# Kernel optimization log

Measured on AMD Instinct MI355X. Metric: run time of the kernel, lower is better.

## Reference

```python
import jax, jax.numpy as jnp
import numpy as np

EMBED = 1024
HEADS = 16
HEAD_DIM = EMBED // HEADS
SCALE = HEAD_DIM ** (-0.5)
LN_EPS = 1e-5


def setup_inputs() -> dict:
    key = jax.random.key(0)
    ks = jax.random.split(key, 8)
    B, N = 2, 2048
    s = EMBED ** -0.5
    return {
        "x": jax.random.normal(ks[0], (B, N, EMBED), dtype=jnp.float32),
        "ln_w": jnp.ones((EMBED,), jnp.float32),
        "ln_b": jnp.zeros((EMBED,), jnp.float32),
        "Wq": jax.random.normal(ks[1], (EMBED, EMBED), jnp.float32) * s,
        "Wk": jax.random.normal(ks[2], (EMBED, EMBED), jnp.float32) * s,
        "Wv": jax.random.normal(ks[3], (EMBED, EMBED), jnp.float32) * s,
        "Wo": jax.random.normal(ks[4], (EMBED, EMBED), jnp.float32) * s,
        "bo": jnp.zeros((EMBED,), jnp.float32),
    }


def reference(x, ln_w, ln_b, Wq, Wk, Wv, Wo, bo):
    residual = x
    # LayerNorm (pre-norm)
    mu = jnp.mean(x, axis=-1, keepdims=True)
    var = jnp.mean(jnp.square(x - mu), axis=-1, keepdims=True)
    xn = (x - mu) * jax.lax.rsqrt(var + LN_EPS) * ln_w + ln_b

    B, N, _ = xn.shape
    q = (xn @ Wq.T).reshape(B, N, HEADS, HEAD_DIM).transpose(0, 2, 1, 3)  # b h n d
    k = (xn @ Wk.T).reshape(B, N, HEADS, HEAD_DIM).transpose(0, 2, 1, 3)
    v = (xn @ Wv.T).reshape(B, N, HEADS, HEAD_DIM).transpose(0, 2, 1, 3)

    dots = jnp.einsum('bhqd,bhkd->bhqk', q, k) * SCALE
    causal = jnp.tril(jnp.ones((N, N), dtype=bool))
    dots = jnp.where(causal, dots, -jnp.inf)
    attn = jax.nn.softmax(dots, axis=-1)
    out = jnp.einsum('bhqk,bhkd->bhqd', attn, v)
    out = out.transpose(0, 2, 1, 3).reshape(B, N, EMBED)
    # dropout is identity in eval mode
    return residual + out @ Wo.T + bo
```

## Files before the change

### kernel.cpp

```cpp
#include <hip/hip_runtime.h>

#define E 1024
#define NSEQ 2048
#define HEADS 16
#define HD 64

typedef unsigned short u16;
typedef short short8 __attribute__((ext_vector_type(8)));
typedef float f32x4 __attribute__((ext_vector_type(4)));

template<bool B> struct BC { static constexpr bool v = B; };

#define GLOAD_LDS16(gp, lp)                                        \
    __builtin_amdgcn_global_load_lds(                              \
        (const __attribute__((address_space(1))) void*)(gp),       \
        (__attribute__((address_space(3))) void*)(lp), 16, 0, 0)

__device__ __forceinline__ u16 f2bf(float f) {
    union { float f; unsigned u; } v; v.f = f;
    unsigned r = v.u + 0x7fffu + ((v.u >> 16) & 1u);
    return (u16)(r >> 16);
}

__device__ __forceinline__ unsigned cvt_pk_bf16(float lo, float hi) {
    unsigned r;
    asm("v_cvt_pk_bf16_f32 %0, %1, %2" : "=v"(r) : "v"(lo), "v"(hi));
    return r;
}

__device__ __forceinline__ f32x4 mfma16(short8 a, short8 b, f32x4 c) {
    return __builtin_amdgcn_mfma_f32_16x16x32_bf16(a, b, c, 0, 0, 0);
}

__global__ __launch_bounds__(256) void prep_k(
    const float* __restrict__ Wq, const float* __restrict__ Wk,
    const float* __restrict__ Wv, const float* __restrict__ Wo,
    const float* __restrict__ X, const float* __restrict__ w,
    const float* __restrict__ bb, u16* __restrict__ Wbf, u16* __restrict__ xn)
{
    if (blockIdx.x < 4096) {
        const unsigned i = (blockIdx.x * 256u + threadIdx.x) * 4u;
        const unsigned m = i >> 20;
        const float* src = (m == 0) ? Wq : (m == 1) ? Wk : (m == 2) ? Wv : Wo;
        const float4 v = *(const float4*)(src + (i & 0xFFFFFu));
        *(uint2*)(Wbf + i) = make_uint2(
            ((unsigned)f2bf(v.x)) | (((unsigned)f2bf(v.y)) << 16),
            ((unsigned)f2bf(v.z)) | (((unsigned)f2bf(v.w)) << 16));
        return;
    }
    const int row = blockIdx.x - 4096, tid = threadIdx.x;
    const int lane = tid & 63, wave = tid >> 6;
    const float4 v = ((const float4*)(X + (size_t)row * E))[tid];
    float s = v.x + v.y + v.z + v.w;
    float s2 = v.x * v.x + v.y * v.y + v.z * v.z + v.w * v.w;
#pragma unroll
    for (int off = 1; off < 64; off <<= 1) {
        s += __shfl_xor(s, off);
        s2 += __shfl_xor(s2, off);
    }
    __shared__ float red[8];
    if (lane == 0) { red[wave] = s; red[4 + wave] = s2; }
    __syncthreads();
    s = red[0] + red[1] + red[2] + red[3];
    s2 = red[4] + red[5] + red[6] + red[7];
    const float mu = s * (1.f / 1024.f);
    float var = s2 * (1.f / 1024.f) - mu * mu;
    var = fmaxf(var, 0.f);
    const float rs = rsqrtf(var + 1e-5f);
    const float4 wv = ((const float4*)w)[tid];
    const float4 bv = ((const float4*)bb)[tid];
    u16 o0 = f2bf((v.x - mu) * rs * wv.x + bv.x);
    u16 o1 = f2bf((v.y - mu) * rs * wv.y + bv.y);
    u16 o2 = f2bf((v.z - mu) * rs * wv.z + bv.z);
    u16 o3 = f2bf((v.w - mu) * rs * wv.w + bv.w);
    *(uint2*)(xn + (size_t)row * E + tid * 4) =
        make_uint2(((unsigned)o0) | (((unsigned)o1) << 16),
                   ((unsigned)o2) | (((unsigned)o3) << 16));
}

__global__ __launch_bounds__(256) void vtrans(
    const u16* __restrict__ Vb, u16* __restrict__ VT)
{
    __shared__ u16 tl[64][65];
    const int t = threadIdx.x;
    const int ntile = blockIdx.x, bh = blockIdx.y;
    const int b = bh >> 4, h = bh & 15;
    const int n0 = ntile * 64;
    {
        const int nl = t >> 2;
        const u16* src = Vb + ((size_t)b * NSEQ + n0 + nl) * E + h * 64;
#pragma unroll
        for (int u = 0; u < 2; ++u) {
            const int d0 = (t & 3) * 16 + u * 8;
            short8 v = *(const short8*)(src + d0);
#pragma unroll
            for (int j = 0; j < 8; ++j) tl[nl][d0 + j] = (u16)v[j];
        }
    }
    __syncthreads();
    {
        const int d = t >> 2, nc = (t & 3) * 16;
        u16* dst = VT + ((size_t)bh * 64 + d) * NSEQ + n0 + nc;
#pragma unroll
        for (int u = 0; u < 2; ++u) {
            short8 o;
#pragma unroll
            for (int j = 0; j < 8; ++j) o[j] = (short)tl[nc + u * 8 + j][d];
            *(short8*)(dst + u * 8) = o;
        }
    }
}

template<int MODE>
__global__ __launch_bounds__(256) void gemm_nt(
    const u16* __restrict__ A, const u16* __restrict__ Wbase,
    u16* __restrict__ outb, float* __restrict__ outf,
    const float* __restrict__ resid, const float* __restrict__ bias)
{
    __shared__ __align__(16) unsigned char As[128 * 128];
    __shared__ __align__(16) unsigned char Bs[128 * 128];
    const int tid = threadIdx.x;
    const int lane = tid & 63, wave = tid >> 6;
    const int l15 = lane & 15, l4 = lane >> 4;
    const int wm = wave >> 1, wn = wave & 1;
    const int nt = blockIdx.x, mt = blockIdx.y, z = blockIdx.z;
    const u16* Bw = Wbase + (size_t)z * (E * (size_t)E);

    const int lrow8 = lane >> 3;
    const int lchunk = (lane & 7) ^ lrow8;
    const u16* gA = A + (size_t)(mt * 128 + lrow8) * E + lchunk * 8;
    const u16* gB = Bw + (size_t)(nt * 128 + lrow8) * E + lchunk * 8;

    f32x4 acc[4][4] = {};

    for (int kt = 0; kt < 16; ++kt) {
#pragma unroll
        for (int i = 0; i < 4; ++i) {
            const int rb = (i * 4 + wave) * 8;
            GLOAD_LDS16(gA + (size_t)rb * E + kt * 64, As + rb * 128);
            GLOAD_LDS16(gB + (size_t)rb * E + kt * 64, Bs + rb * 128);
        }
        __syncthreads();
#pragma unroll
        for (int ks = 0; ks < 2; ++ks) {
            short8 af[4], bfr[4];
#pragma unroll
            for (int i = 0; i < 4; ++i) {
                int ra = wm * 64 + i * 16 + l15;
                af[i] = *(const short8*)(As + ra * 128 + ((ks * 64 + l4 * 16) ^ ((ra & 7) << 4)));
                int rb2 = wn * 64 + i * 16 + l15;
                bfr[i] = *(const short8*)(Bs + rb2 * 128 + ((ks * 64 + l4 * 16) ^ ((rb2 & 7) << 4)));
            }
#pragma unroll
            for (int i = 0; i < 4; ++i)
#pragma unroll
                for (int j = 0; j < 4; ++j)
                    acc[i][j] = mfma16(af[i], bfr[j], acc[i][j]);
        }
        __syncthreads();
    }

    const int orow0 = mt * 128 + wm * 64, ocol0 = nt * 128 + wn * 64;
    if (MODE == 0) {
        u16* outz = outb + (size_t)z * (4096 * (size_t)E);
        const float osc = (z == 0) ? 0.18033688f : 1.0f;
#pragma unroll
        for (int i = 0; i < 4; ++i)
#pragma unroll
            for (int j = 0; j < 4; ++j)
#pragma unroll
                for (int r = 0; r < 4; ++r) {
                    int row = orow0 + i * 16 + l4 * 4 + r;
                    int col = ocol0 + j * 16 + l15;
                    outz[(size_t)row * E + col] = f2bf(acc[i][j][r] * osc);
                }
    } else {
#pragma unroll
        for (int i = 0; i < 4; ++i)
#pragma unroll
            for (int j = 0; j < 4; ++j)
#pragma unroll
                for (int r = 0; r < 4; ++r) {
                    int row = orow0 + i * 16 + l4 * 4 + r;
                    int col = ocol0 + j * 16 + l15;
                    size_t idx = (size_t)row * E + col;
                    outf[idx] = acc[i][j][r] + resid[idx] + bias[col];
                }
    }
}

__global__ __launch_bounds__(256) void attn_fwd(
    const u16* __restrict__ Q, const u16* __restrict__ K,
    const u16* __restrict__ VT, u16* __restrict__ O)
{
    __shared__ __align__(16) unsigned char Kls[2 * 16384];
    __shared__ __align__(16) unsigned char Vls[2 * 16384];
    __shared__ __align__(16) unsigned char Ps[4 * 4096];
    const int tid = threadIdx.x, lane = tid & 63, wave = tid >> 6;
    const int sub = wave >> 1, par = wave & 1;
    const int l15 = lane & 15, l4 = lane >> 4;
    const int h = blockIdx.x, y = blockIdx.y, b = blockIdx.z;
    const int jj = 31 - (int)y;
    const size_t bbase = (size_t)b * NSEQ * E + h * HD;
    const u16* vt = VT + ((size_t)(b * 16 + h) * 64) * NSEQ;

    unsigned char* Pw = Ps + wave * 4096;
    const int srowK = lane >> 3, kchunk = (lane & 7) ^ srowK;
    const int srowV = lane >> 4, vchunk = (lane & 15) ^ (((wave & 1) << 2) + srowV);

    auto stage = [&](int t, int buf) {
        const u16* Kg = K + bbase + (size_t)(t * 128) * E;
        const u16* vg = vt + t * 128;
        unsigned char* kd = Kls + buf * 16384 + wave * 1024;
        unsigned char* vd = Vls + buf * 16384 + wave * 1024;
#pragma unroll
        for (int i = 0; i < 4; ++i)
            GLOAD_LDS16(Kg + (size_t)(wave * 8 + i * 32 + srowK) * E + kchunk * 8, kd + i * 4096);
#pragma unroll
        for (int i = 0; i < 4; ++i)
            GLOAD_LDS16(vg + (size_t)(wave * 4 + i * 16 + srowV) * NSEQ + vchunk * 8, vd + i * 4096);
    };

    const int qw0 = jj * 64 + sub * 32;
    const int R = (jj >> 1) + 1;

    short8 aq[2][2];
#pragma unroll
    for (int qt = 0; qt < 2; ++qt)
#pragma unroll
        for (int ks = 0; ks < 2; ++ks)
            aq[qt][ks] = *(const short8*)(Q + bbase + (size_t)(qw0 + qt * 16 + l15) * E + ks * 32 + l4 * 8);

    f32x4 accO[2][4] = {};
    float mrow[2] = {-5e29f, -5e29f};
    float lrow[2] = {0.f, 0.f};

    stage(0, 0);
    __syncthreads();

    auto step = [&](int t, auto mc) {
        constexpr bool MASK = decltype(mc)::v;
        const int buf = t & 1;
        if (t + 1 < R) stage(t + 1, buf ^ 1);
        const unsigned char* Kc = Kls + buf * 16384;
        const unsigned char* Vc = Vls + buf * 16384;

        f32x4 s[2][4] = {};
#pragma unroll
        for (int kvt = 0; kvt < 4; ++kvt) {
            const int kr = par * 64 + kvt * 16 + l15;
#pragma unroll
            for (int ks = 0; ks < 2; ++ks) {
                short8 kfr = *(const short8*)(Kc + kr * 128 + ((ks * 64 + l4 * 16) ^ ((kr & 7) << 4)));
                s[0][kvt] = mfma16(kfr, aq[0][ks], s[0][kvt]);
                s[1][kvt] = mfma16(kfr, aq[1][ks], s[1][kvt]);
            }
        }

        if constexpr (MASK) {
#pragma unroll
            for (int qt = 0; qt < 2; ++qt) {
                const int qg = qw0 + qt * 16 + l15;
#pragma unroll
                for (int kvt = 0; kvt < 4; ++kvt)
#pragma unroll
                    for (int r = 0; r < 4; ++r) {
                        int kvg = t * 128 + par * 64 + kvt * 16 + l4 * 4 + r;
                        if (kvg > qg) s[qt][kvt][r] = -1e30f;
                    }
            }
        }

#pragma unroll
        for (int qt = 0; qt < 2; ++qt) {
            float m0 = fmaxf(fmaxf(s[qt][0][0], s[qt][0][1]), fmaxf(s[qt][0][2], s[qt][0][3]));
            float m1 = fmaxf(fmaxf(s[qt][1][0], s[qt][1][1]), fmaxf(s[qt][1][2], s[qt][1][3]));
            float m2 = fmaxf(fmaxf(s[qt][2][0], s[qt][2][1]), fmaxf(s[qt][2][2], s[qt][2][3]));
            float m3 = fmaxf(fmaxf(s[qt][3][0], s[qt][3][1]), fmaxf(s[qt][3][2], s[qt][3][3]));
            float pm = fmaxf(fmaxf(m0, m1), fmaxf(m2, m3));
            if (__any(pm > mrow[qt] + 8.f)) {
                pm = fmaxf(pm, __shfl_xor(pm, 16));
                pm = fmaxf(pm, __shfl_xor(pm, 32));
                const float mn = fmaxf(mrow[qt], pm);
                const float sc = exp2f(mrow[qt] - mn);
                mrow[qt] = mn;
                lrow[qt] *= sc;
#pragma unroll
                for (int r = 0; r < 4; ++r) {
                    float scv = __shfl(sc, l4 * 4 + r);
#pragma unroll
                    for (int dt = 0; dt < 4; ++dt) accO[qt][dt][r] *= scv;
                }
            }
            const int pr = qt * 16 + l15;
            const int sw = (l15 & 7) << 4;
#pragma unroll
            for (int kvt = 0; kvt < 4; ++kvt) {
                float p0 = exp2f(s[qt][kvt][0] - mrow[qt]);
                float p1 = exp2f(s[qt][kvt][1] - mrow[qt]);
                float p2 = exp2f(s[qt][kvt][2] - mrow[qt]);
                float p3 = exp2f(s[qt][kvt][3] - mrow[qt]);
                lrow[qt] += (p0 + p1) + (p2 + p3);
                uint2 pk = make_uint2(cvt_pk_bf16(p0, p1), cvt_pk_bf16(p2, p3));
                *(uint2*)(Pw + pr * 128 + ((kvt * 32 + l4 * 8) ^ sw)) = pk;
            }
        }

#pragma unroll
        for (int ks2 = 0; ks2 < 2; ++ks2) {
            const int cb = ks2 * 64 + l4 * 16;
            short8 pf0 = *(const short8*)(Pw + l15 * 128 + (cb ^ ((l15 & 7) << 4)));
            short8 pf1 = *(const short8*)(Pw + (16 + l15) * 128 + (cb ^ ((l15 & 7) << 4)));
#pragma unroll
            for (int dt = 0; dt < 4; ++dt) {
                const int vr = dt * 16 + l15;
                short8 vfr = *(const short8*)(Vc + vr * 256 + ((par * 128 + cb) ^ ((vr & 7) << 4)));
                accO[0][dt] = mfma16(pf0, vfr, accO[0][dt]);
                accO[1][dt] = mfma16(pf1, vfr, accO[1][dt]);
            }
        }
        __syncthreads();
    };

    for (int t = 0; t + 1 < R; ++t) step(t, BC<false>{});
    step(R - 1, BC<true>{});

    f32x4* Mg = (f32x4*)Kls;
    if (par == 1) {
        f32x4 hd;
        hd[0] = mrow[0]; hd[1] = mrow[1]; hd[2] = lrow[0]; hd[3] = lrow[1];
        Mg[(sub * 9) * 64 + lane] = hd;
#pragma unroll
        for (int qt = 0; qt < 2; ++qt)
#pragma unroll
            for (int dt = 0; dt < 4; ++dt)
                Mg[(sub * 9 + 1 + qt * 4 + dt) * 64 + lane] = accO[qt][dt];
    }
    __syncthreads();
    if (par == 0) {
        f32x4 hd = Mg[(sub * 9) * 64 + lane];
        float scA[2], scB[2];
#pragma unroll
        for (int qt = 0; qt < 2; ++qt) {
            const float mB = hd[qt], lB = hd[2 + qt];
            const float ms = fmaxf(mrow[qt], mB);
            scA[qt] = exp2f(mrow[qt] - ms);
            scB[qt] = exp2f(mB - ms);
            lrow[qt] = lrow[qt] * scA[qt] + lB * scB[qt];
        }
#pragma unroll
        for (int qt = 0; qt < 2; ++qt)
#pragma unroll
            for (int r = 0; r < 4; ++r) {
                float sa = __shfl(scA[qt], l4 * 4 + r);
                float sb = __shfl(scB[qt], l4 * 4 + r);
#pragma unroll
                for (int dt = 0; dt < 4; ++dt) {
                    f32x4 ob = Mg[(sub * 9 + 1 + qt * 4 + dt) * 64 + lane];
                    accO[qt][dt][r] = accO[qt][dt][r] * sa + ob[r] * sb;
                }
            }
        float linv[2];
#pragma unroll
        for (int qt = 0; qt < 2; ++qt) {
            float tl2 = lrow[qt];
            tl2 += __shfl_xor(tl2, 16);
            tl2 += __shfl_xor(tl2, 32);
            linv[qt] = 1.f / tl2;
        }
#pragma unroll
        for (int rt = 0; rt < 2; ++rt)
#pragma unroll
            for (int r = 0; r < 4; ++r) {
                float lq = __shfl(linv[rt], l4 * 4 + r);
                const int qg = qw0 + rt * 16 + l4 * 4 + r;
#pragma unroll
                for (int dt = 0; dt < 4; ++dt)
                    O[bbase + (size_t)qg * E + dt * 16 + l15] = f2bf(accO[rt][dt][r] * lq);
            }
    }
}

extern "C" void kernel_launch(void* const* d_in, const int* in_sizes, int n_in,
                              void* d_out, int out_size, void* d_ws, size_t ws_size,
                              hipStream_t stream)
{
    const float* x    = (const float*)d_in[0];
    const float* ln_w = (const float*)d_in[1];
    const float* ln_b = (const float*)d_in[2];
    const float* Wq   = (const float*)d_in[3];
    const float* Wk   = (const float*)d_in[4];
    const float* Wv   = (const float*)d_in[5];
    const float* Wo   = (const float*)d_in[6];
    const float* bo   = (const float*)d_in[7];
    float* out = (float*)d_out;

    u16* ws  = (u16*)d_ws;
    u16* Wbf = ws;
    u16* xn  = Wbf + (size_t)4 * 1024 * 1024;
    u16* Qb  = xn + (size_t)4096 * 1024;
    u16* Kb  = Qb + (size_t)4096 * 1024;
    u16* Vb  = Kb + (size_t)4096 * 1024;
    u16* Ob  = Vb + (size_t)4096 * 1024;
    u16* VT  = xn;

    prep_k<<<dim3(8192), dim3(256), 0, stream>>>(Wq, Wk, Wv, Wo, x, ln_w, ln_b, Wbf, xn);
    gemm_nt<0><<<dim3(8, 32, 3), dim3(256), 0, stream>>>(
        xn, Wbf, Qb, nullptr, nullptr, nullptr);
    vtrans<<<dim3(32, 32), dim3(256), 0, stream>>>(Vb, VT);
    attn_fwd<<<dim3(16, 32, 2), dim3(256), 0, stream>>>(Qb, Kb, VT, Ob);
    gemm_nt<1><<<dim3(8, 32, 1), dim3(256), 0, stream>>>(
        Ob, Wbf + (size_t)3 * 1024 * 1024, nullptr, out, x, bo);
}
```

Baseline: 122.8 us.

## Fuse V transpose into QKV GEMM epilogue and pair causal strips per attention block

The V projection epilogue now transposes its tile through LDS and writes V^T directly, which removes the separate vtrans kernel and its extra global round trip. The attention kernel launches half as many blocks, and each block processes a short and a long causal query strip (jg and 31-jg) to balance work across blocks. The costs are fewer blocks in flight for attention, a longer serial body per block, and LDS reuse in the GEMM epilogue that depends on the waitcnt ordering being correct.

```diff
diff --git a/kernel.cpp b/kernel.cpp
--- a/kernel.cpp
+++ b/kernel.cpp
@@ -8,6 +8,7 @@
 typedef unsigned short u16;
 typedef short short8 __attribute__((ext_vector_type(8)));
 typedef float f32x4 __attribute__((ext_vector_type(4)));
+typedef u16 u16x4 __attribute__((ext_vector_type(4)));
 
 template<bool B> struct BC { static constexpr bool v = B; };
 
@@ -78,43 +79,10 @@
                    ((unsigned)o2) | (((unsigned)o3) << 16));
 }
 
-__global__ __launch_bounds__(256) void vtrans(
-    const u16* __restrict__ Vb, u16* __restrict__ VT)
-{
-    __shared__ u16 tl[64][65];
-    const int t = threadIdx.x;
-    const int ntile = blockIdx.x, bh = blockIdx.y;
-    const int b = bh >> 4, h = bh & 15;
-    const int n0 = ntile * 64;
-    {
-        const int nl = t >> 2;
-        const u16* src = Vb + ((size_t)b * NSEQ + n0 + nl) * E + h * 64;
-#pragma unroll
-        for (int u = 0; u < 2; ++u) {
-            const int d0 = (t & 3) * 16 + u * 8;
-            short8 v = *(const short8*)(src + d0);
-#pragma unroll
-            for (int j = 0; j < 8; ++j) tl[nl][d0 + j] = (u16)v[j];
-        }
-    }
-    __syncthreads();
-    {
-        const int d = t >> 2, nc = (t & 3) * 16;
-        u16* dst = VT + ((size_t)bh * 64 + d) * NSEQ + n0 + nc;
-#pragma unroll
-        for (int u = 0; u < 2; ++u) {
-            short8 o;
-#pragma unroll
-            for (int j = 0; j < 8; ++j) o[j] = (short)tl[nc + u * 8 + j][d];
-            *(short8*)(dst + u * 8) = o;
-        }
-    }
-}
-
 template<int MODE>
 __global__ __launch_bounds__(256) void gemm_nt(
     const u16* __restrict__ A, const u16* __restrict__ Wbase,
-    u16* __restrict__ outb, float* __restrict__ outf,
+    u16* __restrict__ outb, u16* __restrict__ vtout, float* __restrict__ outf,
     const float* __restrict__ resid, const float* __restrict__ bias)
 {
     __shared__ __align__(16) unsigned char As[128 * 128];
@@ -162,18 +130,42 @@
 
     const int orow0 = mt * 128 + wm * 64, ocol0 = nt * 128 + wn * 64;
     if (MODE == 0) {
-        u16* outz = outb + (size_t)z * (4096 * (size_t)E);
-        const float osc = (z == 0) ? 0.18033688f : 1.0f;
-#pragma unroll
-        for (int i = 0; i < 4; ++i)
-#pragma unroll
-            for (int j = 0; j < 4; ++j)
-#pragma unroll
-                for (int r = 0; r < 4; ++r) {
-                    int row = orow0 + i * 16 + l4 * 4 + r;
-                    int col = ocol0 + j * 16 + l15;
-                    outz[(size_t)row * E + col] = f2bf(acc[i][j][r] * osc);
-                }
+        if (z == 2) {
+            unsigned char* wl = (wave < 2) ? (As + wave * 8192) : (Bs + (wave - 2) * 8192);
+#pragma unroll
+            for (int i = 0; i < 4; ++i)
+#pragma unroll
+                for (int j = 0; j < 4; ++j) {
+                    u16x4 pk;
+#pragma unroll
+                    for (int r = 0; r < 4; ++r) pk[r] = f2bf(acc[i][j][r]);
+                    const int dl = j * 16 + l15;
+                    const int boff = dl * 128 + ((i * 32 + l4 * 8) ^ ((dl & 7) << 4));
+                    *(u16x4*)(wl + boff) = pk;
+                }
+            asm volatile("s_waitcnt lgkmcnt(0)" ::: "memory");
+            const int b2 = mt >> 4, hh = nt * 2 + wn;
+            const int n0 = (mt & 15) * 128 + wm * 64;
+            u16* vrow = vtout + (size_t)((b2 * 16 + hh) * 64 + lane) * NSEQ + n0;
+#pragma unroll
+            for (int c = 0; c < 8; ++c) {
+                short8 vv = *(const short8*)(wl + lane * 128 + ((c * 16) ^ ((lane & 7) << 4)));
+                *(short8*)(vrow + c * 8) = vv;
+            }
+        } else {
+            u16* outz = outb + (size_t)z * (4096 * (size_t)E);
+            const float osc = (z == 0) ? 0.18033688f : 1.0f;
+#pragma unroll
+            for (int i = 0; i < 4; ++i)
+#pragma unroll
+                for (int j = 0; j < 4; ++j)
+#pragma unroll
+                    for (int r = 0; r < 4; ++r) {
+                        int row = orow0 + i * 16 + l4 * 4 + r;
+                        int col = ocol0 + j * 16 + l15;
+                        outz[(size_t)row * E + col] = f2bf(acc[i][j][r] * osc);
+                    }
+        }
     } else {
 #pragma unroll
         for (int i = 0; i < 4; ++i)
@@ -199,8 +191,7 @@
     const int tid = threadIdx.x, lane = tid & 63, wave = tid >> 6;
     const int sub = wave >> 1, par = wave & 1;
     const int l15 = lane & 15, l4 = lane >> 4;
-    const int h = blockIdx.x, y = blockIdx.y, b = blockIdx.z;
-    const int jj = 31 - (int)y;
+    const int h = blockIdx.x, jg = blockIdx.y, b = blockIdx.z;
     const size_t bbase = (size_t)b * NSEQ * E + h * HD;
     const u16* vt = VT + ((size_t)(b * 16 + h) * 64) * NSEQ;
 
@@ -221,164 +212,170 @@
             GLOAD_LDS16(vg + (size_t)(wave * 4 + i * 16 + srowV) * NSEQ + vchunk * 8, vd + i * 4096);
     };
 
-    const int qw0 = jj * 64 + sub * 32;
-    const int R = (jj >> 1) + 1;
-
-    short8 aq[2][2];
-#pragma unroll
-    for (int qt = 0; qt < 2; ++qt)
-#pragma unroll
-        for (int ks = 0; ks < 2; ++ks)
-            aq[qt][ks] = *(const short8*)(Q + bbase + (size_t)(qw0 + qt * 16 + l15) * E + ks * 32 + l4 * 8);
-
-    f32x4 accO[2][4] = {};
-    float mrow[2] = {-5e29f, -5e29f};
-    float lrow[2] = {0.f, 0.f};
-
-    stage(0, 0);
-    __syncthreads();
-
-    auto step = [&](int t, auto mc) {
-        constexpr bool MASK = decltype(mc)::v;
-        const int buf = t & 1;
-        if (t + 1 < R) stage(t + 1, buf ^ 1);
-        const unsigned char* Kc = Kls + buf * 16384;
-        const unsigned char* Vc = Vls + buf * 16384;
-
-        f32x4 s[2][4] = {};
-#pragma unroll
-        for (int kvt = 0; kvt < 4; ++kvt) {
-            const int kr = par * 64 + kvt * 16 + l15;
-#pragma unroll
-            for (int ks = 0; ks < 2; ++ks) {
-                short8 kfr = *(const short8*)(Kc + kr * 128 + ((ks * 64 + l4 * 16) ^ ((kr & 7) << 4)));
-                s[0][kvt] = mfma16(kfr, aq[0][ks], s[0][kvt]);
-                s[1][kvt] = mfma16(kfr, aq[1][ks], s[1][kvt]);
-            }
+    auto run_strip = [&](int jj) {
+        const int qw0 = jj * 64 + sub * 32;
+        const int R = (jj >> 1) + 1;
+
+        short8 aq[2][2];
+#pragma unroll
+        for (int qt = 0; qt < 2; ++qt)
+#pragma unroll
+            for (int ks = 0; ks < 2; ++ks)
+                aq[qt][ks] = *(const short8*)(Q + bbase + (size_t)(qw0 + qt * 16 + l15) * E + ks * 32 + l4 * 8);
+
+        f32x4 accO[2][4] = {};
+        float mrow[2] = {-5e29f, -5e29f};
+        float lrow[2] = {0.f, 0.f};
+
+        stage(0, 0);
+        __syncthreads();
+
+        auto step = [&](int t, auto mc) {
+            constexpr bool MASK = decltype(mc)::v;
+            const int buf = t & 1;
+            if (t + 1 < R) stage(t + 1, buf ^ 1);
+            const unsigned char* Kc = Kls + buf * 16384;
+            const unsigned char* Vc = Vls + buf * 16384;
+
+            f32x4 s[2][4] = {};
+#pragma unroll
+            for (int kvt = 0; kvt < 4; ++kvt) {
+                const int kr = par * 64 + kvt * 16 + l15;
+#pragma unroll
+                for (int ks = 0; ks < 2; ++ks) {
+                    short8 kfr = *(const short8*)(Kc + kr * 128 + ((ks * 64 + l4 * 16) ^ ((kr & 7) << 4)));
+                    s[0][kvt] = mfma16(kfr, aq[0][ks], s[0][kvt]);
+                    s[1][kvt] = mfma16(kfr, aq[1][ks], s[1][kvt]);
+                }
+            }
+
+            if constexpr (MASK) {
+#pragma unroll
+                for (int qt = 0; qt < 2; ++qt) {
+                    const int qg = qw0 + qt * 16 + l15;
+#pragma unroll
+                    for (int kvt = 0; kvt < 4; ++kvt)
+#pragma unroll
+                        for (int r = 0; r < 4; ++r) {
+                            int kvg = t * 128 + par * 64 + kvt * 16 + l4 * 4 + r;
+                            if (kvg > qg) s[qt][kvt][r] = -1e30f;
+                        }
+                }
+            }
+
+#pragma unroll
+            for (int qt = 0; qt < 2; ++qt) {
+                float m0 = fmaxf(fmaxf(s[qt][0][0], s[qt][0][1]), fmaxf(s[qt][0][2], s[qt][0][3]));
+                float m1 = fmaxf(fmaxf(s[qt][1][0], s[qt][1][1]), fmaxf(s[qt][1][2], s[qt][1][3]));
+                float m2 = fmaxf(fmaxf(s[qt][2][0], s[qt][2][1]), fmaxf(s[qt][2][2], s[qt][2][3]));
+                float m3 = fmaxf(fmaxf(s[qt][3][0], s[qt][3][1]), fmaxf(s[qt][3][2], s[qt][3][3]));
+                float pm = fmaxf(fmaxf(m0, m1), fmaxf(m2, m3));
+                if (__any(pm > mrow[qt] + 8.f)) {
+                    pm = fmaxf(pm, __shfl_xor(pm, 16));
+                    pm = fmaxf(pm, __shfl_xor(pm, 32));
+                    const float mn = fmaxf(mrow[qt], pm);
+                    const float sc = exp2f(mrow[qt] - mn);
+                    mrow[qt] = mn;
+                    lrow[qt] *= sc;
+#pragma unroll
+                    for (int r = 0; r < 4; ++r) {
+                        float scv = __shfl(sc, l4 * 4 + r);
+#pragma unroll
+                        for (int dt = 0; dt < 4; ++dt) accO[qt][dt][r] *= scv;
+                    }
+                }
+                const int pr = qt * 16 + l15;
+                const int sw = (l15 & 7) << 4;
+#pragma unroll
+                for (int kvt = 0; kvt < 4; ++kvt) {
+                    float p0 = exp2f(s[qt][kvt][0] - mrow[qt]);
+                    float p1 = exp2f(s[qt][kvt][1] - mrow[qt]);
+                    float p2 = exp2f(s[qt][kvt][2] - mrow[qt]);
+                    float p3 = exp2f(s[qt][kvt][3] - mrow[qt]);
+                    lrow[qt] += (p0 + p1) + (p2 + p3);
+                    uint2 pk = make_uint2(cvt_pk_bf16(p0, p1), cvt_pk_bf16(p2, p3));
+                    *(uint2*)(Pw + pr * 128 + ((kvt * 32 + l4 * 8) ^ sw)) = pk;
+                }
+            }
+
+#pragma unroll
+            for (int ks2 = 0; ks2 < 2; ++ks2) {
+                const int cb = ks2 * 64 + l4 * 16;
+                short8 pf0 = *(const short8*)(Pw + l15 * 128 + (cb ^ ((l15 & 7) << 4)));
+                short8 pf1 = *(const short8*)(Pw + (16 + l15) * 128 + (cb ^ ((l15 & 7) << 4)));
+#pragma unroll
+                for (int dt = 0; dt < 4; ++dt) {
+                    const int vr = dt * 16 + l15;
+                    short8 vfr = *(const short8*)(Vc + vr * 256 + ((par * 128 + cb) ^ ((vr & 7) << 4)));
+                    accO[0][dt] = mfma16(pf0, vfr, accO[0][dt]);
+                    accO[1][dt] = mfma16(pf1, vfr, accO[1][dt]);
+                }
+            }
+            __syncthreads();
+        };
+
+        for (int t = 0; t + 1 < R; ++t) step(t, BC<false>{});
+        step(R - 1, BC<true>{});
+
+        f32x4* Mg = (f32x4*)Kls;
+        if (par == 1) {
+            f32x4 hd;
+            hd[0] = mrow[0]; hd[1] = mrow[1]; hd[2] = lrow[0]; hd[3] = lrow[1];
+            Mg[(sub * 9) * 64 + lane] = hd;
+#pragma unroll
+            for (int qt = 0; qt < 2; ++qt)
+#pragma unroll
+                for (int dt = 0; dt < 4; ++dt)
+                    Mg[(sub * 9 + 1 + qt * 4 + dt) * 64 + lane] = accO[qt][dt];
         }
-
-        if constexpr (MASK) {
+        __syncthreads();
+        if (par == 0) {
+            f32x4 hd = Mg[(sub * 9) * 64 + lane];
+            float scA[2], scB[2];
 #pragma unroll
             for (int qt = 0; qt < 2; ++qt) {
-                const int qg = qw0 + qt * 16 + l15;
-#pragma unroll
-                for (int kvt = 0; kvt < 4; ++kvt)
-#pragma unroll
-                    for (int r = 0; r < 4; ++r) {
-                        int kvg = t * 128 + par * 64 + kvt * 16 + l4 * 4 + r;
-                        if (kvg > qg) s[qt][kvt][r] = -1e30f;
+                const float mB = hd[qt], lB = hd[2 + qt];
+                const float ms = fmaxf(mrow[qt], mB);
+                scA[qt] = exp2f(mrow[qt] - ms);
+                scB[qt] = exp2f(mB - ms);
+                lrow[qt] = lrow[qt] * scA[qt] + lB * scB[qt];
+            }
+#pragma unroll
+            for (int qt = 0; qt < 2; ++qt)
+#pragma unroll
+                for (int r = 0; r < 4; ++r) {
+                    float sa = __shfl(scA[qt], l4 * 4 + r);
+                    float sb = __shfl(scB[qt], l4 * 4 + r);
+#pragma unroll
+                    for (int dt = 0; dt < 4; ++dt) {
+                        f32x4 ob = Mg[(sub * 9 + 1 + qt * 4 + dt) * 64 + lane];
+                        accO[qt][dt][r] = accO[qt][dt][r] * sa + ob[r] * sb;
                     }
-            }
-        }
-
-#pragma unroll
-        for (int qt = 0; qt < 2; ++qt) {
-            float m0 = fmaxf(fmaxf(s[qt][0][0], s[qt][0][1]), fmaxf(s[qt][0][2], s[qt][0][3]));
-            float m1 = fmaxf(fmaxf(s[qt][1][0], s[qt][1][1]), fmaxf(s[qt][1][2], s[qt][1][3]));
-            float m2 = fmaxf(fmaxf(s[qt][2][0], s[qt][2][1]), fmaxf(s[qt][2][2], s[qt][2][3]));
-            float m3 = fmaxf(fmaxf(s[qt][3][0], s[qt][3][1]), fmaxf(s[qt][3][2], s[qt][3][3]));
-            float pm = fmaxf(fmaxf(m0, m1), fmaxf(m2, m3));
-            if (__any(pm > mrow[qt] + 8.f)) {
-                pm = fmaxf(pm, __shfl_xor(pm, 16));
-                pm = fmaxf(pm, __shfl_xor(pm, 32));
-                const float mn = fmaxf(mrow[qt], pm);
-                const float sc = exp2f(mrow[qt] - mn);
-                mrow[qt] = mn;
-                lrow[qt] *= sc;
+                }
+            float linv[2];
+#pragma unroll
+            for (int qt = 0; qt < 2; ++qt) {
+                float tl2 = lrow[qt];
+                tl2 += __shfl_xor(tl2, 16);
+                tl2 += __shfl_xor(tl2, 32);
+                linv[qt] = 1.f / tl2;
+            }
+#pragma unroll
+            for (int rt = 0; rt < 2; ++rt)
 #pragma unroll
                 for (int r = 0; r < 4; ++r) {
-                    float scv = __shfl(sc, l4 * 4 + r);
-#pragma unroll
-                    for (int dt = 0; dt < 4; ++dt) accO[qt][dt][r] *= scv;
-                }
-            }
-            const int pr = qt * 16 + l15;
-            const int sw = (l15 & 7) << 4;
-#pragma unroll
-            for (int kvt = 0; kvt < 4; ++kvt) {
-                float p0 = exp2f(s[qt][kvt][0] - mrow[qt]);
-                float p1 = exp2f(s[qt][kvt][1] - mrow[qt]);
-                float p2 = exp2f(s[qt][kvt][2] - mrow[qt]);
-                float p3 = exp2f(s[qt][kvt][3] - mrow[qt]);
-                lrow[qt] += (p0 + p1) + (p2 + p3);
-                uint2 pk = make_uint2(cvt_pk_bf16(p0, p1), cvt_pk_bf16(p2, p3));
-                *(uint2*)(Pw + pr * 128 + ((kvt * 32 + l4 * 8) ^ sw)) = pk;
-            }
-        }
-
-#pragma unroll
-        for (int ks2 = 0; ks2 < 2; ++ks2) {
-            const int cb = ks2 * 64 + l4 * 16;
-            short8 pf0 = *(const short8*)(Pw + l15 * 128 + (cb ^ ((l15 & 7) << 4)));
-            short8 pf1 = *(const short8*)(Pw + (16 + l15) * 128 + (cb ^ ((l15 & 7) << 4)));
-#pragma unroll
-            for (int dt = 0; dt < 4; ++dt) {
-                const int vr = dt * 16 + l15;
-                short8 vfr = *(const short8*)(Vc + vr * 256 + ((par * 128 + cb) ^ ((vr & 7) << 4)));
-                accO[0][dt] = mfma16(pf0, vfr, accO[0][dt]);
-                accO[1][dt] = mfma16(pf1, vfr, accO[1][dt]);
-            }
+                    float lq = __shfl(linv[rt], l4 * 4 + r);
+                    const int qg = qw0 + rt * 16 + l4 * 4 + r;
+#pragma unroll
+                    for (int dt = 0; dt < 4; ++dt)
+                        O[bbase + (size_t)qg * E + dt * 16 + l15] = f2bf(accO[rt][dt][r] * lq);
+                }
         }
         __syncthreads();
     };
 
-    for (int t = 0; t + 1 < R; ++t) step(t, BC<false>{});
-    step(R - 1, BC<true>{});
-
-    f32x4* Mg = (f32x4*)Kls;
-    if (par == 1) {
-        f32x4 hd;
-        hd[0] = mrow[0]; hd[1] = mrow[1]; hd[2] = lrow[0]; hd[3] = lrow[1];
-        Mg[(sub * 9) * 64 + lane] = hd;
-#pragma unroll
-        for (int qt = 0; qt < 2; ++qt)
-#pragma unroll
-            for (int dt = 0; dt < 4; ++dt)
-                Mg[(sub * 9 + 1 + qt * 4 + dt) * 64 + lane] = accO[qt][dt];
-    }
-    __syncthreads();
-    if (par == 0) {
-        f32x4 hd = Mg[(sub * 9) * 64 + lane];
-        float scA[2], scB[2];
-#pragma unroll
-        for (int qt = 0; qt < 2; ++qt) {
-            const float mB = hd[qt], lB = hd[2 + qt];
-            const float ms = fmaxf(mrow[qt], mB);
-            scA[qt] = exp2f(mrow[qt] - ms);
-            scB[qt] = exp2f(mB - ms);
-            lrow[qt] = lrow[qt] * scA[qt] + lB * scB[qt];
-        }
-#pragma unroll
-        for (int qt = 0; qt < 2; ++qt)
-#pragma unroll
-            for (int r = 0; r < 4; ++r) {
-                float sa = __shfl(scA[qt], l4 * 4 + r);
-                float sb = __shfl(scB[qt], l4 * 4 + r);
-#pragma unroll
-                for (int dt = 0; dt < 4; ++dt) {
-                    f32x4 ob = Mg[(sub * 9 + 1 + qt * 4 + dt) * 64 + lane];
-                    accO[qt][dt][r] = accO[qt][dt][r] * sa + ob[r] * sb;
-                }
-            }
-        float linv[2];
-#pragma unroll
-        for (int qt = 0; qt < 2; ++qt) {
-            float tl2 = lrow[qt];
-            tl2 += __shfl_xor(tl2, 16);
-            tl2 += __shfl_xor(tl2, 32);
-            linv[qt] = 1.f / tl2;
-        }
-#pragma unroll
-        for (int rt = 0; rt < 2; ++rt)
-#pragma unroll
-            for (int r = 0; r < 4; ++r) {
-                float lq = __shfl(linv[rt], l4 * 4 + r);
-                const int qg = qw0 + rt * 16 + l4 * 4 + r;
-#pragma unroll
-                for (int dt = 0; dt < 4; ++dt)
-                    O[bbase + (size_t)qg * E + dt * 16 + l15] = f2bf(accO[rt][dt][r] * lq);
-            }
-    }
+    run_strip(jg);
+    run_strip(31 - jg);
 }
 
 extern "C" void kernel_launch(void* const* d_in, const int* in_sizes, int n_in,
@@ -400,15 +397,13 @@
     u16* xn  = Wbf + (size_t)4 * 1024 * 1024;
     u16* Qb  = xn + (size_t)4096 * 1024;
     u16* Kb  = Qb + (size_t)4096 * 1024;
-    u16* Vb  = Kb + (size_t)4096 * 1024;
-    u16* Ob  = Vb + (size_t)4096 * 1024;
-    u16* VT  = xn;
+    u16* VT  = Kb + (size_t)4096 * 1024;
+    u16* Ob  = VT + (size_t)4096 * 1024;
 
     prep_k<<<dim3(8192), dim3(256), 0, stream>>>(Wq, Wk, Wv, Wo, x, ln_w, ln_b, Wbf, xn);
     gemm_nt<0><<<dim3(8, 32, 3), dim3(256), 0, stream>>>(
-        xn, Wbf, Qb, nullptr, nullptr, nullptr);
-    vtrans<<<dim3(32, 32), dim3(256), 0, stream>>>(Vb, VT);
-    attn_fwd<<<dim3(16, 32, 2), dim3(256), 0, stream>>>(Qb, Kb, VT, Ob);
+        xn, Wbf, Qb, VT, nullptr, nullptr, nullptr);
+    attn_fwd<<<dim3(16, 16, 2), dim3(256), 0, stream>>>(Qb, Kb, VT, Ob);
     gemm_nt<1><<<dim3(8, 32, 1), dim3(256), 0, stream>>>(
-        Ob, Wbf + (size_t)3 * 1024 * 1024, nullptr, out, x, bo);
-}
+        Ob, Wbf + (size_t)3 * 1024 * 1024, nullptr, nullptr, out, x, bo);
+}
```

After: 130.1 us. 1.06x slower.
